# Kernel optimization log

Measured on AMD Instinct MI355X. Metric: run time of the kernel, lower is better.

Reference implementation:

```python
import jax, jax.numpy as jnp
import numpy as np

HIDDEN = 256
GROUPS = 4
GDIM = HIDDEN // GROUPS  # 64


def setup_inputs() -> dict:
    key = jax.random.key(0)
    k1, k2, k3, k4 = jax.random.split(key, 4)
    B, N, P = 8, 300, 32
    x = jax.random.normal(k1, (B, N, P, HIDDEN), dtype=jnp.float32)
    query_content = jax.random.normal(k2, (B, N, HIDDEN), dtype=jnp.float32)
    out_dim = GDIM * GDIM * GROUPS
    # nn.Linear default init: U(-1/sqrt(fan_in), 1/sqrt(fan_in))
    bound = 1.0 / np.sqrt(HIDDEN)
    W_gen = jax.random.uniform(k3, (HIDDEN, out_dim), dtype=jnp.float32, minval=-bound, maxval=bound)
    b_gen = jax.random.uniform(k4, (out_dim,), dtype=jnp.float32, minval=-bound, maxval=bound)
    gamma = jnp.ones((HIDDEN,), dtype=jnp.float32)
    beta = jnp.zeros((HIDDEN,), dtype=jnp.float32)
    return {"x": x, "query_content": query_content, "W_gen": W_gen, "b_gen": b_gen, "gamma": gamma, "beta": beta}


def _layer_norm(h, gamma, beta, eps=1e-5):
    mu = jnp.mean(h, axis=-1, keepdims=True)
    var = jnp.var(h, axis=-1, keepdims=True)
    return (h - mu) * jax.lax.rsqrt(var + eps) * gamma + beta


def reference(x, query_content, W_gen, b_gen, gamma, beta):
    B, N, P, C = x.shape
    # dynamic per-query weights: [B,N,G,gd,gd]
    w = (query_content @ W_gen + b_gen).reshape(B, N, GROUPS, GDIM, GDIM)
    xg = x.reshape(B, N, P, GROUPS, GDIM)
    # mixed[...,p,g,e] = sum_d xg[...,p,g,d] * w[...,g,e,d]  (matmul with W^T)
    mixed = jnp.einsum('bnpgd,bnged->bnpge', xg, w).reshape(B, N, P, C)
    return jax.nn.relu(_layer_norm(mixed, gamma, beta))
```

## Files before the change

kernel.cpp:

```cpp
#include <hip/hip_runtime.h>
#include <hip/hip_bf16.h>

typedef __attribute__((ext_vector_type(4))) float floatx4;
typedef __attribute__((ext_vector_type(8))) short short8;

#define HIDDEN 256
#define NOUT 16384

static __device__ __forceinline__ short bf16bits(float x) {
    __hip_bfloat16 h = __float2bfloat16(x);
    return __builtin_bit_cast(short, h);
}

#define GLDS16(gsrc, ldst) \
    __builtin_amdgcn_global_load_lds((const __attribute__((address_space(1))) void*)(gsrc), \
                                     (__attribute__((address_space(3))) void*)(ldst), 16, 0, 0)

__global__ __launch_bounds__(256) void kPrep(
    const float* __restrict__ Wg, short* __restrict__ WgT,
    const float* __restrict__ qc, short* __restrict__ qcb, int n4)
{
    __shared__ short t[64 * 68];
    const int tid = threadIdx.x;

    if (blockIdx.x < 1024) {
        const int n0 = (blockIdx.x & 255) * 64, k0 = (blockIdx.x >> 8) * 64;
        const int r  = tid >> 4;
        const int c4 = tid & 15;
        #pragma unroll
        for (int i = 0; i < 4; ++i) {
            const int kl = r + i * 16;
            float4 f = *reinterpret_cast<const float4*>(Wg + (size_t)(k0 + kl) * NOUT + n0 + c4 * 4);
            short4 v;
            v.x = bf16bits(f.x); v.y = bf16bits(f.y); v.z = bf16bits(f.z); v.w = bf16bits(f.w);
            *reinterpret_cast<short4*>(&t[kl * 68 + c4 * 4]) = v;
        }
        __syncthreads();
        #pragma unroll
        for (int h = 0; h < 2; ++h) {
            const int id = tid + h * 256;
            const int nl = id >> 3, kc = id & 7;
            short8 v;
            #pragma unroll
            for (int j = 0; j < 8; ++j) v[j] = t[(kc * 8 + j) * 68 + nl];
            *reinterpret_cast<short8*>(WgT + (size_t)(n0 + nl) * HIDDEN + k0 + kc * 8) = v;
        }
    } else {
        const int i = (blockIdx.x - 1024) * 256 + tid;
        if (i < n4) {
            float4 f = reinterpret_cast<const float4*>(qc)[i];
            short4 v;
            v.x = bf16bits(f.x); v.y = bf16bits(f.y); v.z = bf16bits(f.z); v.w = bf16bits(f.w);
            reinterpret_cast<short4*>(qcb)[i] = v;
        }
    }
}

__global__ __launch_bounds__(256) void kA3(
    const short* __restrict__ qcb, const short* __restrict__ WgT,
    const float* __restrict__ bg, short* __restrict__ wdyn, int M)
{
    __shared__ short As[128 * 64];
    __shared__ short Bs[128 * 64];

    const int tid  = threadIdx.x;
    const int wave = tid >> 6, lane = tid & 63;
    const int lq   = lane & 15, quad = lane >> 4;
    const int wm   = wave >> 1, wn = wave & 1;
    const int m0   = blockIdx.x * 128;
    const int n0   = blockIdx.y * 128;

    const short* aSrc[4]; const short* bSrc[4];
    short* aDst[4]; short* bDst[4];
    #pragma unroll
    for (int t = 0; t < 4; ++t) {
        const int chunk = t * 256 + wave * 64 + lane;
        const int row = chunk >> 3, kc = chunk & 7;
        const int kcs = kc ^ (row & 7);
        int rA = m0 + row; if (rA >= M) rA = M - 1;
        aSrc[t] = qcb + (size_t)rA * HIDDEN + kcs * 8;
        bSrc[t] = WgT + (size_t)(n0 + row) * HIDDEN + kcs * 8;
        aDst[t] = &As[(t * 256 + wave * 64) * 8];
        bDst[t] = &Bs[(t * 256 + wave * 64) * 8];
    }

    int aOff[2][4], bOff[2][4];
    #pragma unroll
    for (int ks = 0; ks < 2; ++ks)
        #pragma unroll
        for (int i = 0; i < 4; ++i) {
            const int ra = wm * 64 + i * 16 + lq;
            aOff[ks][i] = ra * 64 + (((ks * 4 + quad) ^ (ra & 7)) * 8);
            const int rb = wn * 64 + i * 16 + lq;
            bOff[ks][i] = rb * 64 + (((ks * 4 + quad) ^ (rb & 7)) * 8);
        }

    floatx4 acc[4][4];
    #pragma unroll
    for (int i = 0; i < 4; ++i)
        #pragma unroll
        for (int j = 0; j < 4; ++j) acc[i][j] = (floatx4){0.f, 0.f, 0.f, 0.f};

    for (int it = 0; it < 4; ++it) {
        #pragma unroll
        for (int t = 0; t < 4; ++t) {
            GLDS16(aSrc[t], aDst[t]);
            GLDS16(bSrc[t], bDst[t]);
            aSrc[t] += 64; bSrc[t] += 64;
        }
        __syncthreads();

        #pragma unroll
        for (int ks = 0; ks < 2; ++ks) {
            short8 a[4], b[4];
            #pragma unroll
            for (int i = 0; i < 4; ++i) a[i] = *reinterpret_cast<const short8*>(&As[aOff[ks][i]]);
            #pragma unroll
            for (int j = 0; j < 4; ++j) b[j] = *reinterpret_cast<const short8*>(&Bs[bOff[ks][j]]);
            #pragma unroll
            for (int i = 0; i < 4; ++i)
                #pragma unroll
                for (int j = 0; j < 4; ++j)
                    acc[i][j] = __builtin_amdgcn_mfma_f32_16x16x32_bf16(a[i], b[j], acc[i][j], 0, 0, 0);
        }
        __syncthreads();
    }

    float bv[4];
    #pragma unroll
    for (int j = 0; j < 4; ++j) bv[j] = bg[n0 + wn * 64 + j * 16 + lq];

    short* Cs = As;
    #pragma unroll
    for (int half = 0; half < 2; ++half) {
        if (half) __syncthreads();
        if (wm == half) {
            #pragma unroll
            for (int j = 0; j < 4; ++j)
                #pragma unroll
                for (int i = 0; i < 4; ++i)
                    #pragma unroll
                    for (int r = 0; r < 4; ++r)
                        Cs[(i * 16 + quad * 4 + r) * 128 + wn * 64 + j * 16 + lq] =
                            bf16bits(acc[i][j][r] + bv[j]);
        }
        __syncthreads();
        #pragma unroll
        for (int t = 0; t < 4; ++t) {
            const int id = t * 256 + tid;
            const int mr = id >> 4, ch = id & 15;
            const int grow = m0 + half * 64 + mr;
            if (grow < M)
                *reinterpret_cast<short8*>(&wdyn[(size_t)grow * NOUT + n0 + ch * 8]) =
                    *reinterpret_cast<const short8*>(&Cs[mr * 128 + ch * 8]);
        }
    }
}

__global__ __launch_bounds__(256) void kB3(
    const float* __restrict__ x, const short* __restrict__ wdyn,
    const float* __restrict__ gamma, const float* __restrict__ beta,
    float* __restrict__ out)
{
    __shared__ float red[2][4][4][2][2];

    const int tid  = threadIdx.x;
    const int bnq  = blockIdx.x;
    const int wave = tid >> 6, lane = tid & 63;
    const int lq   = lane & 15, quad = lane >> 4;
    const int mtile = wave & 1, gp = wave >> 1;

    const float* xr = x + (size_t)bnq * (32 * HIDDEN) + (mtile * 16 + lq) * HIDDEN;
    const short* wr = wdyn + (size_t)bnq * NOUT;

    short8 afr[2][2];
    #pragma unroll
    for (int gi = 0; gi < 2; ++gi) {
        const int g = gp * 2 + gi;
        #pragma unroll
        for (int ks = 0; ks < 2; ++ks) {
            const floatx4* s = reinterpret_cast<const floatx4*>(xr + g * 64 + ks * 32 + quad * 8);
            const floatx4 f0 = __builtin_nontemporal_load(s);
            const floatx4 f1 = __builtin_nontemporal_load(s + 1);
            short8 v;
            v[0]=bf16bits(f0[0]); v[1]=bf16bits(f0[1]); v[2]=bf16bits(f0[2]); v[3]=bf16bits(f0[3]);
            v[4]=bf16bits(f1[0]); v[5]=bf16bits(f1[1]); v[6]=bf16bits(f1[2]); v[7]=bf16bits(f1[3]);
            afr[gi][ks] = v;
        }
    }

    floatx4 acc[2][4];
    #pragma unroll
    for (int gi = 0; gi < 2; ++gi)
        #pragma unroll
        for (int nt = 0; nt < 4; ++nt) acc[gi][nt] = (floatx4){0.f, 0.f, 0.f, 0.f};

    #pragma unroll
    for (int gi = 0; gi < 2; ++gi) {
        const int g = gp * 2 + gi;
        #pragma unroll
        for (int ks = 0; ks < 2; ++ks) {
            #pragma unroll
            for (int nt = 0; nt < 4; ++nt) {
                const short8 b = __builtin_nontemporal_load(reinterpret_cast<const short8*>(
                    wr + (g * 64 + nt * 16 + lq) * 64 + ks * 32 + quad * 8));
                acc[gi][nt] = __builtin_amdgcn_mfma_f32_16x16x32_bf16(afr[gi][ks], b, acc[gi][nt], 0, 0, 0);
            }
        }
    }

    float s[4], ss[4];
    #pragma unroll
    for (int r = 0; r < 4; ++r) { s[r] = 0.f; ss[r] = 0.f; }
    #pragma unroll
    for (int gi = 0; gi < 2; ++gi)
        #pragma unroll
        for (int nt = 0; nt < 4; ++nt)
            #pragma unroll
            for (int r = 0; r < 4; ++r) {
                const float v = acc[gi][nt][r];
                s[r] += v; ss[r] += v * v;
            }
    #pragma unroll
    for (int off = 1; off < 16; off <<= 1) {
        #pragma unroll
        for (int r = 0; r < 4; ++r) {
            s[r]  += __shfl_xor(s[r],  off);
            ss[r] += __shfl_xor(ss[r], off);
        }
    }
    if (lq == 0) {
        #pragma unroll
        for (int r = 0; r < 4; ++r) {
            red[mtile][quad][r][gp][0] = s[r];
            red[mtile][quad][r][gp][1] = ss[r];
        }
    }
    __syncthreads();

    float mu[4], rs[4];
    #pragma unroll
    for (int r = 0; r < 4; ++r) {
        const float S  = s[r]  + red[mtile][quad][r][gp ^ 1][0];
        const float SS = ss[r] + red[mtile][quad][r][gp ^ 1][1];
        mu[r] = S * (1.f / 256.f);
        float var = SS * (1.f / 256.f) - mu[r] * mu[r];
        var = fmaxf(var, 0.f);
        rs[r] = rsqrtf(var + 1e-5f);
    }

    float* orow = out + (size_t)bnq * (32 * HIDDEN);
    #pragma unroll
    for (int gi = 0; gi < 2; ++gi) {
        const int g = gp * 2 + gi;
        #pragma unroll
        for (int nt = 0; nt < 4; ++nt) {
            const int c = g * 64 + nt * 16 + lq;
            const float gm = gamma[c], bt = beta[c];
            #pragma unroll
            for (int r = 0; r < 4; ++r) {
                const int p = mtile * 16 + quad * 4 + r;
                const float v = fmaxf((acc[gi][nt][r] - mu[r]) * rs[r] * gm + bt, 0.f);
                __builtin_nontemporal_store(v, &orow[p * HIDDEN + c]);
            }
        }
    }
}

extern "C" void kernel_launch(void* const* d_in, const int* in_sizes, int n_in,
                              void* d_out, int out_size, void* d_ws, size_t ws_size,
                              hipStream_t stream)
{
    const float* x     = (const float*)d_in[0];
    const float* qc    = (const float*)d_in[1];
    const float* Wg    = (const float*)d_in[2];
    const float* bg    = (const float*)d_in[3];
    const float* gamma = (const float*)d_in[4];
    const float* beta  = (const float*)d_in[5];
    float* out = (float*)d_out;

    const int M = in_sizes[1] / HIDDEN;

    char* ws = (char*)d_ws;
    short* wdyn = (short*)ws;
    short* WgT  = (short*)(ws + (size_t)M * NOUT * 2);
    short* qcb  = (short*)(ws + (size_t)M * NOUT * 2 + (size_t)NOUT * HIDDEN * 2);

    const int n4 = (M * HIDDEN) / 4;
    const int prepBlocks = 1024 + (n4 + 255) / 256;
    kPrep<<<prepBlocks, 256, 0, stream>>>(Wg, WgT, qc, qcb, n4);

    kA3<<<dim3((M + 127) / 128, NOUT / 128), 256, 0, stream>>>(qcb, WgT, bg, wdyn, M);

    kB3<<<M, 256, 0, stream>>>(x, wdyn, gamma, beta, out);
}
```

Before: 237.6 us.

## Permute generated weight columns so kB reads fragments contiguously; drop LDS staging in kA

```diff
diff --git a/kernel.cpp b/kernel.cpp
--- a/kernel.cpp
+++ b/kernel.cpp
@@ -12,12 +12,19 @@
     return __builtin_bit_cast(short, h);
 }
 
-#define GLDS16(gsrc, ldst) \
-    __builtin_amdgcn_global_load_lds((const __attribute__((address_space(1))) void*)(gsrc), \
-                                     (__attribute__((address_space(3))) void*)(ldst), 16, 0, 0)
+static __device__ __forceinline__ int permc(int c) {
+    const int g = c >> 12, e = (c >> 6) & 63, d = c & 63;
+    const int nt = e >> 4, lq = e & 15, ks = (d >> 5) & 1, quad = (d >> 3) & 3, j = d & 7;
+    return ((((g << 2) | nt) << 1 | ks) << 9) | (((quad << 4) | lq) << 3) | j;
+}
+static __device__ __forceinline__ int invperm(int p) {
+    const int blk = p >> 9, g = blk >> 3, nt = (blk >> 1) & 3, ks = blk & 1;
+    const int r = (p >> 3) & 63, quad = r >> 4, lq = r & 15, j = p & 7;
+    return g * 4096 + (nt * 16 + lq) * 64 + ks * 32 + quad * 8 + j;
+}
 
 __global__ __launch_bounds__(256) void kPrep(
-    const float* __restrict__ Wg, short* __restrict__ WgT,
+    const float* __restrict__ Wg, short* __restrict__ WgTp,
     const float* __restrict__ qc, short* __restrict__ qcb, int n4)
 {
     __shared__ short t[64 * 68];
@@ -43,7 +50,8 @@
             short8 v;
             #pragma unroll
             for (int j = 0; j < 8; ++j) v[j] = t[(kc * 8 + j) * 68 + nl];
-            *reinterpret_cast<short8*>(WgT + (size_t)(n0 + nl) * HIDDEN + k0 + kc * 8) = v;
+            const int prow = permc(n0 + nl);
+            *reinterpret_cast<short8*>(WgTp + (size_t)prow * HIDDEN + k0 + kc * 8) = v;
         }
     } else {
         const int i = (blockIdx.x - 1024) * 256 + tid;
@@ -56,12 +64,11 @@
     }
 }
 
-__global__ __launch_bounds__(256) void kA3(
-    const short* __restrict__ qcb, const short* __restrict__ WgT,
+__global__ __launch_bounds__(256) void kA4(
+    const short* __restrict__ qcb, const short* __restrict__ WgTp,
     const float* __restrict__ bg, short* __restrict__ wdyn, int M)
 {
-    __shared__ short As[128 * 64];
-    __shared__ short Bs[128 * 64];
+    __shared__ short Cs[64 * 128];
 
     const int tid  = threadIdx.x;
     const int wave = tid >> 6, lane = tid & 63;
@@ -70,30 +77,14 @@
     const int m0   = blockIdx.x * 128;
     const int n0   = blockIdx.y * 128;
 
-    const short* aSrc[4]; const short* bSrc[4];
-    short* aDst[4]; short* bDst[4];
-    #pragma unroll
-    for (int t = 0; t < 4; ++t) {
-        const int chunk = t * 256 + wave * 64 + lane;
-        const int row = chunk >> 3, kc = chunk & 7;
-        const int kcs = kc ^ (row & 7);
-        int rA = m0 + row; if (rA >= M) rA = M - 1;
-        aSrc[t] = qcb + (size_t)rA * HIDDEN + kcs * 8;
-        bSrc[t] = WgT + (size_t)(n0 + row) * HIDDEN + kcs * 8;
-        aDst[t] = &As[(t * 256 + wave * 64) * 8];
-        bDst[t] = &Bs[(t * 256 + wave * 64) * 8];
-    }
-
-    int aOff[2][4], bOff[2][4];
-    #pragma unroll
-    for (int ks = 0; ks < 2; ++ks)
-        #pragma unroll
-        for (int i = 0; i < 4; ++i) {
-            const int ra = wm * 64 + i * 16 + lq;
-            aOff[ks][i] = ra * 64 + (((ks * 4 + quad) ^ (ra & 7)) * 8);
-            const int rb = wn * 64 + i * 16 + lq;
-            bOff[ks][i] = rb * 64 + (((ks * 4 + quad) ^ (rb & 7)) * 8);
-        }
+    const short* aP[4];
+    const short* bP[4];
+    #pragma unroll
+    for (int i = 0; i < 4; ++i) {
+        int ra = m0 + wm * 64 + i * 16 + lq; if (ra >= M) ra = M - 1;
+        aP[i] = qcb  + (size_t)ra * HIDDEN + quad * 8;
+        bP[i] = WgTp + (size_t)(n0 + wn * 64 + i * 16 + lq) * HIDDEN + quad * 8;
+    }
 
     floatx4 acc[4][4];
     #pragma unroll
@@ -101,39 +92,27 @@
         #pragma unroll
         for (int j = 0; j < 4; ++j) acc[i][j] = (floatx4){0.f, 0.f, 0.f, 0.f};
 
-    for (int it = 0; it < 4; ++it) {
-        #pragma unroll
-        for (int t = 0; t < 4; ++t) {
-            GLDS16(aSrc[t], aDst[t]);
-            GLDS16(bSrc[t], bDst[t]);
-            aSrc[t] += 64; bSrc[t] += 64;
-        }
+    #pragma unroll
+    for (int s = 0; s < 8; ++s) {
+        short8 a[4], b[4];
+        #pragma unroll
+        for (int i = 0; i < 4; ++i) a[i] = *reinterpret_cast<const short8*>(aP[i] + s * 32);
+        #pragma unroll
+        for (int j = 0; j < 4; ++j) b[j] = *reinterpret_cast<const short8*>(bP[j] + s * 32);
+        #pragma unroll
+        for (int i = 0; i < 4; ++i)
+            #pragma unroll
+            for (int j = 0; j < 4; ++j)
+                acc[i][j] = __builtin_amdgcn_mfma_f32_16x16x32_bf16(a[i], b[j], acc[i][j], 0, 0, 0);
+    }
+
+    float bv[4];
+    #pragma unroll
+    for (int j = 0; j < 4; ++j) bv[j] = bg[invperm(n0 + wn * 64 + j * 16 + lq)];
+
+    #pragma unroll
+    for (int half = 0; half < 2; ++half) {
         __syncthreads();
-
-        #pragma unroll
-        for (int ks = 0; ks < 2; ++ks) {
-            short8 a[4], b[4];
-            #pragma unroll
-            for (int i = 0; i < 4; ++i) a[i] = *reinterpret_cast<const short8*>(&As[aOff[ks][i]]);
-            #pragma unroll
-            for (int j = 0; j < 4; ++j) b[j] = *reinterpret_cast<const short8*>(&Bs[bOff[ks][j]]);
-            #pragma unroll
-            for (int i = 0; i < 4; ++i)
-                #pragma unroll
-                for (int j = 0; j < 4; ++j)
-                    acc[i][j] = __builtin_amdgcn_mfma_f32_16x16x32_bf16(a[i], b[j], acc[i][j], 0, 0, 0);
-        }
-        __syncthreads();
-    }
-
-    float bv[4];
-    #pragma unroll
-    for (int j = 0; j < 4; ++j) bv[j] = bg[n0 + wn * 64 + j * 16 + lq];
-
-    short* Cs = As;
-    #pragma unroll
-    for (int half = 0; half < 2; ++half) {
-        if (half) __syncthreads();
         if (wm == half) {
             #pragma unroll
             for (int j = 0; j < 4; ++j)
@@ -157,7 +136,7 @@
     }
 }
 
-__global__ __launch_bounds__(256) void kB3(
+__global__ __launch_bounds__(256) void kB4(
     const float* __restrict__ x, const short* __restrict__ wdyn,
     const float* __restrict__ gamma, const float* __restrict__ beta,
     float* __restrict__ out)
@@ -202,8 +181,8 @@
         for (int ks = 0; ks < 2; ++ks) {
             #pragma unroll
             for (int nt = 0; nt < 4; ++nt) {
-                const short8 b = __builtin_nontemporal_load(reinterpret_cast<const short8*>(
-                    wr + (g * 64 + nt * 16 + lq) * 64 + ks * 32 + quad * 8));
+                const short8 b = *reinterpret_cast<const short8*>(
+                    wr + (((((g << 2) | nt) << 1) | ks) << 9) + lane * 8);
                 acc[gi][nt] = __builtin_amdgcn_mfma_f32_16x16x32_bf16(afr[gi][ks], b, acc[gi][nt], 0, 0, 0);
             }
         }
@@ -283,14 +262,14 @@
 
     char* ws = (char*)d_ws;
     short* wdyn = (short*)ws;
-    short* WgT  = (short*)(ws + (size_t)M * NOUT * 2);
+    short* WgTp = (short*)(ws + (size_t)M * NOUT * 2);
     short* qcb  = (short*)(ws + (size_t)M * NOUT * 2 + (size_t)NOUT * HIDDEN * 2);
 
     const int n4 = (M * HIDDEN) / 4;
     const int prepBlocks = 1024 + (n4 + 255) / 256;
-    kPrep<<<prepBlocks, 256, 0, stream>>>(Wg, WgT, qc, qcb, n4);
-
-    kA3<<<dim3((M + 127) / 128, NOUT / 128), 256, 0, stream>>>(qcb, WgT, bg, wdyn, M);
-
-    kB3<<<M, 256, 0, stream>>>(x, wdyn, gamma, beta, out);
-}
+    kPrep<<<prepBlocks, 256, 0, stream>>>(Wg, WgTp, qc, qcb, n4);
+
+    kA4<<<dim3((M + 127) / 128, NOUT / 128), 256, 0, stream>>>(qcb, WgTp, bg, wdyn, M);
+
+    kB4<<<M, 256, 0, stream>>>(x, wdyn, gamma, beta, out);
+}
```

Result: slower. 263.5 us (+10.9%).

## Permute generated weight columns so dynamic weights are stored in MFMA fragment order

Applied to the files above, without the earlier changes.

```diff
diff --git a/kernel.cpp b/kernel.cpp
--- a/kernel.cpp
+++ b/kernel.cpp
@@ -16,8 +16,19 @@
     __builtin_amdgcn_global_load_lds((const __attribute__((address_space(1))) void*)(gsrc), \
                                      (__attribute__((address_space(3))) void*)(ldst), 16, 0, 0)
 
+static __device__ __forceinline__ int permc(int c) {
+    const int g = c >> 12, e = (c >> 6) & 63, d = c & 63;
+    const int nt = e >> 4, lq = e & 15, ks = (d >> 5) & 1, quad = (d >> 3) & 3, j = d & 7;
+    return ((((g << 2) | nt) << 1 | ks) << 9) | (((quad << 4) | lq) << 3) | j;
+}
+static __device__ __forceinline__ int invperm(int p) {
+    const int blk = p >> 9, g = blk >> 3, nt = (blk >> 1) & 3, ks = blk & 1;
+    const int r = (p >> 3) & 63, quad = r >> 4, lq = r & 15, j = p & 7;
+    return g * 4096 + (nt * 16 + lq) * 64 + ks * 32 + quad * 8 + j;
+}
+
 __global__ __launch_bounds__(256) void kPrep(
-    const float* __restrict__ Wg, short* __restrict__ WgT,
+    const float* __restrict__ Wg, short* __restrict__ WgTp,
     const float* __restrict__ qc, short* __restrict__ qcb, int n4)
 {
     __shared__ short t[64 * 68];
@@ -43,7 +54,8 @@
             short8 v;
             #pragma unroll
             for (int j = 0; j < 8; ++j) v[j] = t[(kc * 8 + j) * 68 + nl];
-            *reinterpret_cast<short8*>(WgT + (size_t)(n0 + nl) * HIDDEN + k0 + kc * 8) = v;
+            const int prow = permc(n0 + nl);
+            *reinterpret_cast<short8*>(WgTp + (size_t)prow * HIDDEN + k0 + kc * 8) = v;
         }
     } else {
         const int i = (blockIdx.x - 1024) * 256 + tid;
@@ -56,8 +68,8 @@
     }
 }
 
-__global__ __launch_bounds__(256) void kA3(
-    const short* __restrict__ qcb, const short* __restrict__ WgT,
+__global__ __launch_bounds__(256) void kA5(
+    const short* __restrict__ qcb, const short* __restrict__ WgTp,
     const float* __restrict__ bg, short* __restrict__ wdyn, int M)
 {
     __shared__ short As[128 * 64];
@@ -78,8 +90,8 @@
         const int row = chunk >> 3, kc = chunk & 7;
         const int kcs = kc ^ (row & 7);
         int rA = m0 + row; if (rA >= M) rA = M - 1;
-        aSrc[t] = qcb + (size_t)rA * HIDDEN + kcs * 8;
-        bSrc[t] = WgT + (size_t)(n0 + row) * HIDDEN + kcs * 8;
+        aSrc[t] = qcb  + (size_t)rA * HIDDEN + kcs * 8;
+        bSrc[t] = WgTp + (size_t)(n0 + row) * HIDDEN + kcs * 8;
         aDst[t] = &As[(t * 256 + wave * 64) * 8];
         bDst[t] = &Bs[(t * 256 + wave * 64) * 8];
     }
@@ -128,7 +140,7 @@
 
     float bv[4];
     #pragma unroll
-    for (int j = 0; j < 4; ++j) bv[j] = bg[n0 + wn * 64 + j * 16 + lq];
+    for (int j = 0; j < 4; ++j) bv[j] = bg[invperm(n0 + wn * 64 + j * 16 + lq)];
 
     short* Cs = As;
     #pragma unroll
@@ -157,7 +169,7 @@
     }
 }
 
-__global__ __launch_bounds__(256) void kB3(
+__global__ __launch_bounds__(256) void kB4(
     const float* __restrict__ x, const short* __restrict__ wdyn,
     const float* __restrict__ gamma, const float* __restrict__ beta,
     float* __restrict__ out)
@@ -202,8 +214,8 @@
         for (int ks = 0; ks < 2; ++ks) {
             #pragma unroll
             for (int nt = 0; nt < 4; ++nt) {
-                const short8 b = __builtin_nontemporal_load(reinterpret_cast<const short8*>(
-                    wr + (g * 64 + nt * 16 + lq) * 64 + ks * 32 + quad * 8));
+                const short8 b = *reinterpret_cast<const short8*>(
+                    wr + (((((g << 2) | nt) << 1) | ks) << 9) + lane * 8);
                 acc[gi][nt] = __builtin_amdgcn_mfma_f32_16x16x32_bf16(afr[gi][ks], b, acc[gi][nt], 0, 0, 0);
             }
         }
@@ -283,14 +295,14 @@
 
     char* ws = (char*)d_ws;
     short* wdyn = (short*)ws;
-    short* WgT  = (short*)(ws + (size_t)M * NOUT * 2);
+    short* WgTp = (short*)(ws + (size_t)M * NOUT * 2);
     short* qcb  = (short*)(ws + (size_t)M * NOUT * 2 + (size_t)NOUT * HIDDEN * 2);
 
     const int n4 = (M * HIDDEN) / 4;
     const int prepBlocks = 1024 + (n4 + 255) / 256;
-    kPrep<<<prepBlocks, 256, 0, stream>>>(Wg, WgT, qc, qcb, n4);
-
-    kA3<<<dim3((M + 127) / 128, NOUT / 128), 256, 0, stream>>>(qcb, WgT, bg, wdyn, M);
-
-    kB3<<<M, 256, 0, stream>>>(x, wdyn, gamma, beta, out);
-}
+    kPrep<<<prepBlocks, 256, 0, stream>>>(Wg, WgTp, qc, qcb, n4);
+
+    kA5<<<dim3((M + 127) / 128, NOUT / 128), 256, 0, stream>>>(qcb, WgTp, bg, wdyn, M);
+
+    kB4<<<M, 256, 0, stream>>>(x, wdyn, gamma, beta, out);
+}
```

Measured after the change: 221.6 us. -6.8%, faster.
